# Optimization experiments

Measured on AMD Instinct MI355X. Metric: run time of the kernel, lower is better.

Reference implementation:

```python
import jax, jax.numpy as jnp
import numpy as np

NUM_GRAPHS = 1024

def setup_inputs() -> dict:
    key = jax.random.key(0)
    k1, k2, k3, k4 = jax.random.split(key, 4)
    N, D, H = 200000, 512, 128
    h = jax.random.normal(k1, (N, D), dtype=jnp.float32)
    batch = jnp.sort(jax.random.randint(k2, (N,), 0, NUM_GRAPHS)).astype(jnp.int32)
    # gate MLP params: Linear(D,H) -> tanh -> Linear(H,1)
    W1 = jax.random.normal(k3, (D, H), dtype=jnp.float32) / np.sqrt(D)
    b1 = jnp.zeros((H,), dtype=jnp.float32)
    W2 = jax.random.normal(k4, (H, 1), dtype=jnp.float32) / np.sqrt(H)
    b2 = jnp.zeros((1,), dtype=jnp.float32)
    return {"h": h, "batch": batch, "W1": W1, "b1": b1, "W2": W2, "b2": b2}

def reference(h, batch, W1, b1, W2, b2):
    # gate MLP -> per-node logit
    logits = (jnp.tanh(h @ W1 + b1) @ W2 + b2)[:, 0]  # [N]
    # segment softmax over nodes within each graph
    seg_max = jax.ops.segment_max(logits, batch, num_segments=NUM_GRAPHS,
                                  indices_are_sorted=True)  # [G]
    ex = jnp.exp(logits - seg_max[batch])  # [N]
    denom = jax.ops.segment_sum(ex, batch, num_segments=NUM_GRAPHS,
                                indices_are_sorted=True)  # [G]
    a = ex / denom[batch]  # [N]
    # weighted scatter-add pooling
    pooled = jax.ops.segment_sum(h * a[:, None], batch, num_segments=NUM_GRAPHS,
                                 indices_are_sorted=True)  # [G, D]
    return pooled
```

## Files before the change

kernel.cpp:

```cpp
#include <hip/hip_runtime.h>
#include <hip/hip_bf16.h>

typedef __attribute__((ext_vector_type(8))) short short8;
typedef __attribute__((ext_vector_type(4))) float f32x4;

#define NGRAPHS 1024
#define D_DIM 512
#define H_DIM 128
#define BM 64

static __device__ __forceinline__ unsigned int pack_bf2(float a, float b) {
    float2 t; t.x = a; t.y = b;
    __hip_bfloat162 h = __float22bfloat162_rn(t);
    union { __hip_bfloat162 h; unsigned int u; } v;
    v.h = h;
    return v.u;
}

static __device__ __forceinline__ unsigned short f2bf(float f) {
    __hip_bfloat16 h = __float2bfloat16(f);
    union { __hip_bfloat16 h; unsigned short u; } v;
    v.h = h;
    return v.u;
}

static __device__ __forceinline__ float fast_tanh(float x) {
    float cx = fminf(fmaxf(x, -15.f), 15.f);
    float e = __expf(2.f * cx);
    return (e - 1.f) / (e + 1.f);
}

__global__ void seg_offsets_kernel(const int* __restrict__ batch, int N,
                                   int* __restrict__ off) {
    int g = blockIdx.x * 256 + threadIdx.x;
    if (g > NGRAPHS) return;
    int lo = 0, hi = N;
    while (lo < hi) {
        int mid = (lo + hi) >> 1;
        if (batch[mid] < g) lo = mid + 1;
        else hi = mid;
    }
    off[g] = lo;
}

__global__ void prep_w1t_kernel(const float* __restrict__ W1,
                                unsigned short* __restrict__ W1TF) {
    int idx = blockIdx.x * 256 + threadIdx.x;
    int e = idx & 7;
    int lane = (idx >> 3) & 63;
    int ki = (idx >> 9) & 15;
    int cgrp = idx >> 13;
    int col = cgrp * 16 + (lane & 15);
    int k = ki * 32 + (lane >> 4) * 8 + e;
    W1TF[idx] = f2bf(W1[k * H_DIM + col]);
}

__global__ __launch_bounds__(512) void gate_pool_partial_kernel(
    const float* __restrict__ h, const unsigned short* __restrict__ W1TF,
    const float* __restrict__ b1, const float* __restrict__ W2,
    const int* __restrict__ batch, float* __restrict__ P,
    float* __restrict__ out, int N) {
    __shared__ unsigned short hA[BM * D_DIM];
    __shared__ float plds[8][BM];
    __shared__ float wl[BM];
    __shared__ int gb[BM];

    const int tid = threadIdx.x;
    const int lane = tid & 63;
    const int w = tid >> 6;
    const int cg = lane & 15;
    const int qg = lane >> 4;
    const int row0 = blockIdx.x * BM;

    if (tid < BM) {
        int gr = row0 + tid;
        gb[tid] = batch[gr < N ? gr : N - 1];
    }

    {
        float4 f[16];
#pragma unroll
        for (int i = 0; i < 16; ++i) {
            const int task = i * 8 + w;
            const int row = task >> 1, half = task & 1;
            int gr = row0 + row;
            gr = gr < N ? gr : N - 1;
            f[i] = *(const float4*)(h + (size_t)gr * D_DIM + half * 256 + lane * 4);
        }
        __builtin_amdgcn_sched_barrier(0);
#pragma unroll
        for (int i = 0; i < 16; ++i) {
            const int task = i * 8 + w;
            const int row = task >> 1, half = task & 1;
            const int unit = half * 32 + (lane >> 1);
            uint2 v;
            v.x = pack_bf2(f[i].x, f[i].y);
            v.y = pack_bf2(f[i].z, f[i].w);
            *(uint2*)&hA[row * D_DIM + ((unit ^ (row & 7)) * 8) + (lane & 1) * 4] = v;
        }
    }

    short8 bfr[16];
#pragma unroll
    for (int ki = 0; ki < 16; ++ki)
        bfr[ki] = *(const short8*)(W1TF + ((w * 16 + ki) << 9) + lane * 8);
    __syncthreads();

    f32x4 acc[4];
#pragma unroll
    for (int rf = 0; rf < 4; ++rf) acc[rf] = (f32x4){0.f, 0.f, 0.f, 0.f};
#pragma unroll
    for (int ki = 0; ki < 16; ++ki) {
#pragma unroll
        for (int rf = 0; rf < 4; ++rf) {
            const short8 af = *(const short8*)&hA[(rf * 16 + cg) * D_DIM +
                (((4 * ki + qg) ^ (cg & 7)) * 8)];
            acc[rf] = __builtin_amdgcn_mfma_f32_16x16x32_bf16(af, bfr[ki],
                                                              acc[rf], 0, 0, 0);
        }
    }

    const float b1v = b1[w * 16 + cg];
    const float w2v = W2[w * 16 + cg];
#pragma unroll
    for (int rf = 0; rf < 4; ++rf) {
#pragma unroll
        for (int reg = 0; reg < 4; ++reg) {
            float p = fast_tanh(acc[rf][reg] + b1v) * w2v;
#pragma unroll
            for (int o = 1; o < 16; o <<= 1) p += __shfl_xor(p, o, 64);
            if (cg == 0) plds[w][rf * 16 + qg * 4 + reg] = p;
        }
    }
    __syncthreads();

    if (tid < BM) {
        float l = plds[0][tid] + plds[1][tid] + plds[2][tid] + plds[3][tid] +
                  plds[4][tid] + plds[5][tid] + plds[6][tid] + plds[7][tid];
        wl[tid] = (row0 + tid < N) ? __expf(fminf(l, 60.f)) : 0.f;
    }
    __syncthreads();

    {
        const int unit0 = tid >> 3;
        const int e = tid & 7;
        float ax = 0.f, d = 0.f;
        int curg = gb[0];
#pragma unroll 8
        for (int j = 0; j < BM; ++j) {
            const int gj = gb[j];
            if (gj != curg) {
                if (curg == gb[0]) {
                    float* rec = P + (size_t)blockIdx.x * 2 * 513;
                    rec[tid] = ax;
                    if (tid == 0) rec[512] = d;
                } else {
                    out[(size_t)curg * D_DIM + tid] = ax / d;
                }
                ax = 0.f; d = 0.f; curg = gj;
            }
            const float wj = wl[j];
            const unsigned short us =
                hA[j * D_DIM + ((unit0 ^ (j & 7)) * 8) + e];
            ax += wj * __uint_as_float(((unsigned int)us) << 16);
            d += wj;
        }
        {
            const int slot = (curg == gb[0]) ? 0 : 1;
            float* rec = P + ((size_t)blockIdx.x * 2 + slot) * 513;
            rec[tid] = ax;
            if (tid == 0) rec[512] = d;
        }
        if (gb[0] == gb[BM - 1]) {
            float* r1 = P + ((size_t)blockIdx.x * 2 + 1) * 513;
            r1[tid] = 0.f;
            if (tid == 0) r1[512] = 0.f;
        }
    }
}

__global__ __launch_bounds__(512) void reduce_kernel(
    const float* __restrict__ P, const int* __restrict__ off,
    const int* __restrict__ batch, float* __restrict__ out, int N) {
    const int g = blockIdx.x;
    const int tid = threadIdx.x;
    const int s = off[g], e = off[g + 1];
    if (e <= s) { out[(size_t)g * D_DIM + tid] = 0.f; return; }
    const int t0 = s >> 6, t1 = (e - 1) >> 6;
    float sum = 0.f, den = 0.f;
    bool found = false;
    for (int b = t0; b <= t1; ++b) {
        const int fg = batch[b << 6];
        const int le = (b << 6) + 63;
        const int lg = batch[le < N ? le : N - 1];
        if (fg == g) {
            const float* rec = P + (size_t)b * 2 * 513;
            sum += rec[tid]; den += rec[512]; found = true;
        } else if (lg == g) {
            const float* rec = P + ((size_t)b * 2 + 1) * 513;
            sum += rec[tid]; den += rec[512]; found = true;
        }
    }
    if (found) out[(size_t)g * D_DIM + tid] = sum / den;
}

__global__ void zero_kernel(float* __restrict__ out, float* __restrict__ den) {
    int i = blockIdx.x * 256 + threadIdx.x;
    if (i < NGRAPHS * D_DIM) out[i] = 0.f;
    if (i < NGRAPHS) den[i] = 0.f;
}

__global__ __launch_bounds__(256) void gate_pool_atomic_kernel(
    const float* __restrict__ h, const unsigned short* __restrict__ W1TF,
    const float* __restrict__ b1, const float* __restrict__ W2,
    const int* __restrict__ batch, float* __restrict__ outnum,
    float* __restrict__ den, int N) {
    __shared__ unsigned short hA[BM * D_DIM];
    __shared__ float plds[4][BM];
    __shared__ float wl[BM];
    __shared__ int gb[BM];

    const int tid = threadIdx.x;
    const int lane = tid & 63;
    const int w = tid >> 6;
    const int cg = lane & 15;
    const int qg = lane >> 4;
    const int row0 = blockIdx.x * BM;

    if (tid < BM) {
        int gr = row0 + tid;
        gb[tid] = batch[gr < N ? gr : N - 1];
    }
#pragma unroll
    for (int b = 0; b < 4; ++b) {
        float4 fa[4], fb[4];
#pragma unroll
        for (int i = 0; i < 4; ++i) {
            const int fi = (b * 4 + i) * 256 + tid;
            const int r = fi >> 6, u = fi & 63;
            int gr = row0 + r;
            gr = gr < N ? gr : N - 1;
            const float* p = h + (size_t)gr * D_DIM + u * 8;
            fa[i] = *(const float4*)p;
            fb[i] = *(const float4*)(p + 4);
        }
#pragma unroll
        for (int i = 0; i < 4; ++i) {
            const int fi = (b * 4 + i) * 256 + tid;
            const int r = fi >> 6, u = fi & 63;
            uint4 val;
            val.x = pack_bf2(fa[i].x, fa[i].y);
            val.y = pack_bf2(fa[i].z, fa[i].w);
            val.z = pack_bf2(fb[i].x, fb[i].y);
            val.w = pack_bf2(fb[i].z, fb[i].w);
            *(uint4*)&hA[r * D_DIM + ((u ^ (r & 7)) * 8)] = val;
        }
    }
    __syncthreads();

    f32x4 acc[4][2];
#pragma unroll
    for (int rf = 0; rf < 4; ++rf)
#pragma unroll
        for (int cf = 0; cf < 2; ++cf) acc[rf][cf] = (f32x4){0.f, 0.f, 0.f, 0.f};
#pragma unroll
    for (int ki = 0; ki < 16; ++ki) {
        short8 bfg[2];
#pragma unroll
        for (int cf = 0; cf < 2; ++cf)
            bfg[cf] = *(const short8*)(W1TF + (((w * 2 + cf) * 16 + ki) << 9) + lane * 8);
#pragma unroll
        for (int rf = 0; rf < 4; ++rf) {
            const int row = rf * 16 + cg;
            const short8 af = *(const short8*)&hA[row * D_DIM +
                (((4 * ki + qg) ^ (row & 7)) * 8)];
#pragma unroll
            for (int cf = 0; cf < 2; ++cf)
                acc[rf][cf] = __builtin_amdgcn_mfma_f32_16x16x32_bf16(
                    af, bfg[cf], acc[rf][cf], 0, 0, 0);
        }
    }
    const float b1v0 = b1[w * 32 + cg];
    const float b1v1 = b1[w * 32 + 16 + cg];
    const float w2v0 = W2[w * 32 + cg];
    const float w2v1 = W2[w * 32 + 16 + cg];
#pragma unroll
    for (int rf = 0; rf < 4; ++rf) {
#pragma unroll
        for (int reg = 0; reg < 4; ++reg) {
            float p = fast_tanh(acc[rf][0][reg] + b1v0) * w2v0 +
                      fast_tanh(acc[rf][1][reg] + b1v1) * w2v1;
#pragma unroll
            for (int o = 1; o < 16; o <<= 1) p += __shfl_xor(p, o, 64);
            if (cg == 0) plds[w][rf * 16 + qg * 4 + reg] = p;
        }
    }
    __syncthreads();
    if (tid < BM) {
        const float l = plds[0][tid] + plds[1][tid] + plds[2][tid] + plds[3][tid];
        wl[tid] = (row0 + tid < N) ? __expf(fminf(l, 60.f)) : 0.f;
    }
    __syncthreads();

    const int d0 = (tid >> 2) * 8 + (tid & 3) * 2;
    float ax = 0.f, ay = 0.f;
    int cur = gb[0];
#pragma unroll 8
    for (int j = 0; j < BM; ++j) {
        const int gj = gb[j];
        if (gj != cur) {
            atomicAdd(&outnum[(size_t)cur * D_DIM + d0], ax);
            atomicAdd(&outnum[(size_t)cur * D_DIM + d0 + 1], ay);
            ax = 0.f; ay = 0.f; cur = gj;
        }
        const float wj = wl[j];
        const unsigned int pair = *(const unsigned int*)&hA[j * D_DIM +
            (((tid >> 2) ^ (j & 7)) * 8) + (tid & 3) * 2];
        ax += wj * __uint_as_float(pair << 16);
        ay += wj * __uint_as_float(pair & 0xffff0000u);
    }
    atomicAdd(&outnum[(size_t)cur * D_DIM + d0], ax);
    atomicAdd(&outnum[(size_t)cur * D_DIM + d0 + 1], ay);

    if (tid == 0) {
        float a = 0.f;
        int c2 = gb[0];
        for (int j = 0; j < BM; ++j) {
            if (gb[j] != c2) { atomicAdd(&den[c2], a); a = 0.f; c2 = gb[j]; }
            a += wl[j];
        }
        atomicAdd(&den[c2], a);
    }
}

__global__ __launch_bounds__(512) void finalize_kernel(
    float* __restrict__ out, const float* __restrict__ den) {
    const int g = blockIdx.x;
    const float dv = den[g];
    const float v = out[(size_t)g * D_DIM + threadIdx.x];
    out[(size_t)g * D_DIM + threadIdx.x] = dv > 0.f ? v / dv : 0.f;
}

extern "C" void kernel_launch(void* const* d_in, const int* in_sizes, int n_in,
                              void* d_out, int out_size, void* d_ws, size_t ws_size,
                              hipStream_t stream) {
    const float* h = (const float*)d_in[0];
    const int* batch = (const int*)d_in[1];
    const float* W1 = (const float*)d_in[2];
    const float* b1 = (const float*)d_in[3];
    const float* W2 = (const float*)d_in[4];
    float* out = (float*)d_out;
    const int N = in_sizes[1];
    const int NB = (N + BM - 1) / BM;

    char* ws = (char*)d_ws;
    int* off = (int*)ws;
    unsigned short* W1TF = (unsigned short*)(ws + 4608);
    float* P = (float*)(ws + 135680);

    const size_t need = 135680 + (size_t)NB * 2 * 513 * 4;

    seg_offsets_kernel<<<(NGRAPHS + 256) / 256 + 1, 256, 0, stream>>>(batch, N, off);
    prep_w1t_kernel<<<(D_DIM * H_DIM) / 256, 256, 0, stream>>>(W1, W1TF);

    if (ws_size >= need) {
        gate_pool_partial_kernel<<<NB, 512, 0, stream>>>(h, W1TF, b1, W2, batch,
                                                         P, out, N);
        reduce_kernel<<<NGRAPHS, 512, 0, stream>>>(P, off, batch, out, N);
    } else {
        float* den = P;
        zero_kernel<<<(NGRAPHS * D_DIM + 255) / 256, 256, 0, stream>>>(out, den);
        gate_pool_atomic_kernel<<<NB, 256, 0, stream>>>(h, W1TF, b1, W2, batch,
                                                        out, den, N);
        finalize_kernel<<<NGRAPHS, 512, 0, stream>>>(out, den);
    }
}
```

Baseline: 155.6 us.

## Halve gate-pool block to 256 threads with two column fragments per wave

Cuts the partial gate/pool kernel from 512 to 256 threads with launch bounds allowing two blocks per CU. Each wave now computes two 16-column MFMA fragments with swapped operands, so the tanh/W2 reduction is done mostly in-register with only two cross-lane shuffles instead of four per value. The pooling loop reads bf16 pairs so each thread accumulates two features. The aim is less shuffle and sync overhead and more overlap between blocks, at the cost of more registers per thread and about 64KB of LDS per block, which may limit residency.

```diff
diff --git a/kernel.cpp b/kernel.cpp
--- a/kernel.cpp
+++ b/kernel.cpp
@@ -55,13 +55,13 @@
     W1TF[idx] = f2bf(W1[k * H_DIM + col]);
 }
 
-__global__ __launch_bounds__(512) void gate_pool_partial_kernel(
+__global__ __launch_bounds__(256, 2) void gate_pool_partial_kernel(
     const float* __restrict__ h, const unsigned short* __restrict__ W1TF,
     const float* __restrict__ b1, const float* __restrict__ W2,
     const int* __restrict__ batch, float* __restrict__ P,
     float* __restrict__ out, int N) {
     __shared__ unsigned short hA[BM * D_DIM];
-    __shared__ float plds[8][BM];
+    __shared__ float plds[4][BM];
     __shared__ float wl[BM];
     __shared__ int gb[BM];
 
@@ -77,11 +77,12 @@
         gb[tid] = batch[gr < N ? gr : N - 1];
     }
 
-    {
+#pragma unroll
+    for (int bb = 0; bb < 2; ++bb) {
         float4 f[16];
 #pragma unroll
         for (int i = 0; i < 16; ++i) {
-            const int task = i * 8 + w;
+            const int task = (bb * 16 + i) * 4 + w;
             const int row = task >> 1, half = task & 1;
             int gr = row0 + row;
             gr = gr < N ? gr : N - 1;
@@ -90,7 +91,7 @@
         __builtin_amdgcn_sched_barrier(0);
 #pragma unroll
         for (int i = 0; i < 16; ++i) {
-            const int task = i * 8 + w;
+            const int task = (bb * 16 + i) * 4 + w;
             const int row = task >> 1, half = task & 1;
             const int unit = half * 32 + (lane >> 1);
             uint2 v;
@@ -100,51 +101,64 @@
         }
     }
 
-    short8 bfr[16];
-#pragma unroll
-    for (int ki = 0; ki < 16; ++ki)
-        bfr[ki] = *(const short8*)(W1TF + ((w * 16 + ki) << 9) + lane * 8);
-    __syncthreads();
-
-    f32x4 acc[4];
-#pragma unroll
-    for (int rf = 0; rf < 4; ++rf) acc[rf] = (f32x4){0.f, 0.f, 0.f, 0.f};
+    short8 bfr[2][16];
+#pragma unroll
+    for (int cf = 0; cf < 2; ++cf)
+#pragma unroll
+        for (int ki = 0; ki < 16; ++ki)
+            bfr[cf][ki] = *(const short8*)(W1TF +
+                (((w * 2 + cf) * 16 + ki) << 9) + lane * 8);
+    __syncthreads();
+
+    f32x4 acc[4][2];
+#pragma unroll
+    for (int rf = 0; rf < 4; ++rf)
+#pragma unroll
+        for (int cf = 0; cf < 2; ++cf) acc[rf][cf] = (f32x4){0.f, 0.f, 0.f, 0.f};
 #pragma unroll
     for (int ki = 0; ki < 16; ++ki) {
 #pragma unroll
         for (int rf = 0; rf < 4; ++rf) {
             const short8 af = *(const short8*)&hA[(rf * 16 + cg) * D_DIM +
                 (((4 * ki + qg) ^ (cg & 7)) * 8)];
-            acc[rf] = __builtin_amdgcn_mfma_f32_16x16x32_bf16(af, bfr[ki],
-                                                              acc[rf], 0, 0, 0);
-        }
-    }
-
-    const float b1v = b1[w * 16 + cg];
-    const float w2v = W2[w * 16 + cg];
+#pragma unroll
+            for (int cf = 0; cf < 2; ++cf)
+                acc[rf][cf] = __builtin_amdgcn_mfma_f32_16x16x32_bf16(
+                    bfr[cf][ki], af, acc[rf][cf], 0, 0, 0);
+        }
+    }
+
+    float4 b1v[2], w2v[2];
+#pragma unroll
+    for (int cf = 0; cf < 2; ++cf) {
+        b1v[cf] = *(const float4*)&b1[w * 32 + cf * 16 + qg * 4];
+        w2v[cf] = *(const float4*)&W2[w * 32 + cf * 16 + qg * 4];
+    }
 #pragma unroll
     for (int rf = 0; rf < 4; ++rf) {
-#pragma unroll
-        for (int reg = 0; reg < 4; ++reg) {
-            float p = fast_tanh(acc[rf][reg] + b1v) * w2v;
-#pragma unroll
-            for (int o = 1; o < 16; o <<= 1) p += __shfl_xor(p, o, 64);
-            if (cg == 0) plds[w][rf * 16 + qg * 4 + reg] = p;
-        }
+        float p = 0.f;
+#pragma unroll
+        for (int cf = 0; cf < 2; ++cf) {
+            p += fast_tanh(acc[rf][cf][0] + b1v[cf].x) * w2v[cf].x;
+            p += fast_tanh(acc[rf][cf][1] + b1v[cf].y) * w2v[cf].y;
+            p += fast_tanh(acc[rf][cf][2] + b1v[cf].z) * w2v[cf].z;
+            p += fast_tanh(acc[rf][cf][3] + b1v[cf].w) * w2v[cf].w;
+        }
+        p += __shfl_xor(p, 16, 64);
+        p += __shfl_xor(p, 32, 64);
+        if (qg == 0) plds[w][rf * 16 + cg] = p;
     }
     __syncthreads();
 
     if (tid < BM) {
-        float l = plds[0][tid] + plds[1][tid] + plds[2][tid] + plds[3][tid] +
-                  plds[4][tid] + plds[5][tid] + plds[6][tid] + plds[7][tid];
+        const float l = plds[0][tid] + plds[1][tid] + plds[2][tid] + plds[3][tid];
         wl[tid] = (row0 + tid < N) ? __expf(fminf(l, 60.f)) : 0.f;
     }
     __syncthreads();
 
     {
-        const int unit0 = tid >> 3;
-        const int e = tid & 7;
-        float ax = 0.f, d = 0.f;
+        const int d0 = (tid >> 2) * 8 + (tid & 3) * 2;
+        float ax = 0.f, ay = 0.f, d = 0.f;
         int curg = gb[0];
 #pragma unroll 8
         for (int j = 0; j < BM; ++j) {
@@ -152,28 +166,28 @@
             if (gj != curg) {
                 if (curg == gb[0]) {
                     float* rec = P + (size_t)blockIdx.x * 2 * 513;
-                    rec[tid] = ax;
+                    rec[d0] = ax; rec[d0 + 1] = ay;
                     if (tid == 0) rec[512] = d;
                 } else {
-                    out[(size_t)curg * D_DIM + tid] = ax / d;
+                    out[(size_t)curg * D_DIM + d0] = ax / d;
+                    out[(size_t)curg * D_DIM + d0 + 1] = ay / d;
                 }
-                ax = 0.f; d = 0.f; curg = gj;
+                ax = 0.f; ay = 0.f; d = 0.f; curg = gj;
             }
             const float wj = wl[j];
-            const unsigned short us =
-                hA[j * D_DIM + ((unit0 ^ (j & 7)) * 8) + e];
-            ax += wj * __uint_as_float(((unsigned int)us) << 16);
+            const unsigned int pair = *(const unsigned int*)&hA[j * D_DIM +
+                (((tid >> 2) ^ (j & 7)) * 8) + (tid & 3) * 2];
+            ax += wj * __uint_as_float(pair << 16);
+            ay += wj * __uint_as_float(pair & 0xffff0000u);
             d += wj;
         }
-        {
-            const int slot = (curg == gb[0]) ? 0 : 1;
-            float* rec = P + ((size_t)blockIdx.x * 2 + slot) * 513;
-            rec[tid] = ax;
-            if (tid == 0) rec[512] = d;
-        }
+        const int slot = (curg == gb[0]) ? 0 : 1;
+        float* rec = P + ((size_t)blockIdx.x * 2 + slot) * 513;
+        rec[d0] = ax; rec[d0 + 1] = ay;
+        if (tid == 0) rec[512] = d;
         if (gb[0] == gb[BM - 1]) {
             float* r1 = P + ((size_t)blockIdx.x * 2 + 1) * 513;
-            r1[tid] = 0.f;
+            r1[d0] = 0.f; r1[d0 + 1] = 0.f;
             if (tid == 0) r1[512] = 0.f;
         }
     }
@@ -364,7 +378,7 @@
     prep_w1t_kernel<<<(D_DIM * H_DIM) / 256, 256, 0, stream>>>(W1, W1TF);
 
     if (ws_size >= need) {
-        gate_pool_partial_kernel<<<NB, 512, 0, stream>>>(h, W1TF, b1, W2, batch,
+        gate_pool_partial_kernel<<<NB, 256, 0, stream>>>(h, W1TF, b1, W2, batch,
                                                          P, out, N);
         reduce_kernel<<<NGRAPHS, 512, 0, stream>>>(P, off, batch, out, N);
     } else {
```

Measured after the change: 137.7 us (median of 2 runs). 1.13x faster.

## Halve partial-kernel row tile to 32 and swap MFMA operand order for gate epilogue

Applied to the files above, without the earlier changes.

Shrinks the per-block row tile of the partial pooling kernel from 64 to 32 rows. This halves LDS use and register arrays and lets more blocks fit per CU (launch_bounds 512,4), at the cost of twice as many blocks and partial records for the reduce kernel. It also swaps the MFMA A/B operands so each lane holds four consecutive hidden columns. That lets the tanh·W2 epilogue sum four values in-lane and needs only two cross-lane shuffles instead of four per value. The atomic fallback keeps a separate 64-row tile constant.

```diff
diff --git a/kernel.cpp b/kernel.cpp
--- a/kernel.cpp
+++ b/kernel.cpp
@@ -7,7 +7,8 @@
 #define NGRAPHS 1024
 #define D_DIM 512
 #define H_DIM 128
-#define BM 64
+#define BM 32
+#define BMA 64
 
 static __device__ __forceinline__ unsigned int pack_bf2(float a, float b) {
     float2 t; t.x = a; t.y = b;
@@ -55,7 +56,7 @@
     W1TF[idx] = f2bf(W1[k * H_DIM + col]);
 }
 
-__global__ __launch_bounds__(512) void gate_pool_partial_kernel(
+__global__ __launch_bounds__(512, 4) void gate_pool_partial_kernel(
     const float* __restrict__ h, const unsigned short* __restrict__ W1TF,
     const float* __restrict__ b1, const float* __restrict__ W2,
     const int* __restrict__ batch, float* __restrict__ P,
@@ -78,9 +79,9 @@
     }
 
     {
-        float4 f[16];
-#pragma unroll
-        for (int i = 0; i < 16; ++i) {
+        float4 f[8];
+#pragma unroll
+        for (int i = 0; i < 8; ++i) {
             const int task = i * 8 + w;
             const int row = task >> 1, half = task & 1;
             int gr = row0 + row;
@@ -89,7 +90,7 @@
         }
         __builtin_amdgcn_sched_barrier(0);
 #pragma unroll
-        for (int i = 0; i < 16; ++i) {
+        for (int i = 0; i < 8; ++i) {
             const int task = i * 8 + w;
             const int row = task >> 1, half = task & 1;
             const int unit = half * 32 + (lane >> 1);
@@ -106,31 +107,31 @@
         bfr[ki] = *(const short8*)(W1TF + ((w * 16 + ki) << 9) + lane * 8);
     __syncthreads();
 
-    f32x4 acc[4];
-#pragma unroll
-    for (int rf = 0; rf < 4; ++rf) acc[rf] = (f32x4){0.f, 0.f, 0.f, 0.f};
+    f32x4 acc[2];
+    acc[0] = (f32x4){0.f, 0.f, 0.f, 0.f};
+    acc[1] = (f32x4){0.f, 0.f, 0.f, 0.f};
 #pragma unroll
     for (int ki = 0; ki < 16; ++ki) {
 #pragma unroll
-        for (int rf = 0; rf < 4; ++rf) {
+        for (int rf = 0; rf < 2; ++rf) {
             const short8 af = *(const short8*)&hA[(rf * 16 + cg) * D_DIM +
                 (((4 * ki + qg) ^ (cg & 7)) * 8)];
-            acc[rf] = __builtin_amdgcn_mfma_f32_16x16x32_bf16(af, bfr[ki],
-                                                              acc[rf], 0, 0, 0);
-        }
-    }
-
-    const float b1v = b1[w * 16 + cg];
-    const float w2v = W2[w * 16 + cg];
-#pragma unroll
-    for (int rf = 0; rf < 4; ++rf) {
-#pragma unroll
-        for (int reg = 0; reg < 4; ++reg) {
-            float p = fast_tanh(acc[rf][reg] + b1v) * w2v;
-#pragma unroll
-            for (int o = 1; o < 16; o <<= 1) p += __shfl_xor(p, o, 64);
-            if (cg == 0) plds[w][rf * 16 + qg * 4 + reg] = p;
-        }
+            acc[rf] = __builtin_amdgcn_mfma_f32_16x16x32_bf16(
+                bfr[ki], af, acc[rf], 0, 0, 0);
+        }
+    }
+
+    const float4 b1v = *(const float4*)&b1[w * 16 + qg * 4];
+    const float4 w2v = *(const float4*)&W2[w * 16 + qg * 4];
+#pragma unroll
+    for (int rf = 0; rf < 2; ++rf) {
+        float p = fast_tanh(acc[rf][0] + b1v.x) * w2v.x +
+                  fast_tanh(acc[rf][1] + b1v.y) * w2v.y +
+                  fast_tanh(acc[rf][2] + b1v.z) * w2v.z +
+                  fast_tanh(acc[rf][3] + b1v.w) * w2v.w;
+        p += __shfl_xor(p, 16, 64);
+        p += __shfl_xor(p, 32, 64);
+        if (qg == 0) plds[w][rf * 16 + cg] = p;
     }
     __syncthreads();
 
@@ -165,12 +166,10 @@
             ax += wj * __uint_as_float(((unsigned int)us) << 16);
             d += wj;
         }
-        {
-            const int slot = (curg == gb[0]) ? 0 : 1;
-            float* rec = P + ((size_t)blockIdx.x * 2 + slot) * 513;
-            rec[tid] = ax;
-            if (tid == 0) rec[512] = d;
-        }
+        const int slot = (curg == gb[0]) ? 0 : 1;
+        float* rec = P + ((size_t)blockIdx.x * 2 + slot) * 513;
+        rec[tid] = ax;
+        if (tid == 0) rec[512] = d;
         if (gb[0] == gb[BM - 1]) {
             float* r1 = P + ((size_t)blockIdx.x * 2 + 1) * 513;
             r1[tid] = 0.f;
@@ -186,12 +185,12 @@
     const int tid = threadIdx.x;
     const int s = off[g], e = off[g + 1];
     if (e <= s) { out[(size_t)g * D_DIM + tid] = 0.f; return; }
-    const int t0 = s >> 6, t1 = (e - 1) >> 6;
+    const int t0 = s >> 5, t1 = (e - 1) >> 5;
     float sum = 0.f, den = 0.f;
     bool found = false;
     for (int b = t0; b <= t1; ++b) {
-        const int fg = batch[b << 6];
-        const int le = (b << 6) + 63;
+        const int fg = batch[b << 5];
+        const int le = (b << 5) + 31;
         const int lg = batch[le < N ? le : N - 1];
         if (fg == g) {
             const float* rec = P + (size_t)b * 2 * 513;
@@ -215,19 +214,19 @@
     const float* __restrict__ b1, const float* __restrict__ W2,
     const int* __restrict__ batch, float* __restrict__ outnum,
     float* __restrict__ den, int N) {
-    __shared__ unsigned short hA[BM * D_DIM];
-    __shared__ float plds[4][BM];
-    __shared__ float wl[BM];
-    __shared__ int gb[BM];
+    __shared__ unsigned short hA[BMA * D_DIM];
+    __shared__ float plds[4][BMA];
+    __shared__ float wl[BMA];
+    __shared__ int gb[BMA];
 
     const int tid = threadIdx.x;
     const int lane = tid & 63;
     const int w = tid >> 6;
     const int cg = lane & 15;
     const int qg = lane >> 4;
-    const int row0 = blockIdx.x * BM;
-
-    if (tid < BM) {
+    const int row0 = blockIdx.x * BMA;
+
+    if (tid < BMA) {
         int gr = row0 + tid;
         gb[tid] = batch[gr < N ? gr : N - 1];
     }
@@ -296,7 +295,7 @@
         }
     }
     __syncthreads();
-    if (tid < BM) {
+    if (tid < BMA) {
         const float l = plds[0][tid] + plds[1][tid] + plds[2][tid] + plds[3][tid];
         wl[tid] = (row0 + tid < N) ? __expf(fminf(l, 60.f)) : 0.f;
     }
@@ -306,7 +305,7 @@
     float ax = 0.f, ay = 0.f;
     int cur = gb[0];
 #pragma unroll 8
-    for (int j = 0; j < BM; ++j) {
+    for (int j = 0; j < BMA; ++j) {
         const int gj = gb[j];
         if (gj != cur) {
             atomicAdd(&outnum[(size_t)cur * D_DIM + d0], ax);
@@ -325,7 +324,7 @@
     if (tid == 0) {
         float a = 0.f;
         int c2 = gb[0];
-        for (int j = 0; j < BM; ++j) {
+        for (int j = 0; j < BMA; ++j) {
             if (gb[j] != c2) { atomicAdd(&den[c2], a); a = 0.f; c2 = gb[j]; }
             a += wl[j];
         }
@@ -370,8 +369,8 @@
     } else {
         float* den = P;
         zero_kernel<<<(NGRAPHS * D_DIM + 255) / 256, 256, 0, stream>>>(out, den);
-        gate_pool_atomic_kernel<<<NB, 256, 0, stream>>>(h, W1TF, b1, W2, batch,
-                                                        out, den, N);
+        gate_pool_atomic_kernel<<<(N + BMA - 1) / BMA, 256, 0, stream>>>(
+            h, W1TF, b1, W2, batch, out, den, N);
         finalize_kernel<<<NGRAPHS, 512, 0, stream>>>(out, den);
     }
 }
```

Result: faster. 140.4 us (-9.8%).
